# Kernel tuning notes

Hardware: AMD Instinct MI355X
Metric: run time of the kernel (lower is better)

Reference implementation:

```python
import jax, jax.numpy as jnp
import numpy as np

N_NODES = 50000
N_EDGES = 800000
D = 256          # in/out/hidden channels
F_EDGE = 64      # edge feature dim (edge_attr_dim - 1)
LN_EPS = 1e-5


def setup_inputs() -> dict:
    key = jax.random.key(0)
    ks = jax.random.split(key, 12)
    s = 0.05
    return {
        "x": jax.random.normal(ks[0], (N_NODES, D), jnp.float32),
        "edge_index": jax.random.randint(ks[1], (2, N_EDGES), 0, N_NODES, jnp.int64),
        "edge_attr": jax.random.normal(ks[2], (N_EDGES, F_EDGE + 1), jnp.float32),
        "W_e1": jax.random.normal(ks[3], (D, F_EDGE), jnp.float32) * s,
        "b_e1": jnp.zeros((D,), jnp.float32),
        "W_e2": jax.random.normal(ks[4], (D, D), jnp.float32) * s,
        "b_e2": jnp.zeros((D,), jnp.float32),
        "W_le": jax.random.normal(ks[5], (D, D), jnp.float32) * s,
        "b_le": jnp.zeros((D,), jnp.float32),
        "W_g1": jax.random.normal(ks[6], (D, D), jnp.float32) * s,
        "b_g1": jnp.zeros((D,), jnp.float32),
        "ln_g": jnp.ones((D,), jnp.float32),
        "ln_b": jnp.zeros((D,), jnp.float32),
        "W_g2": jax.random.normal(ks[7], (D, D), jnp.float32) * s,
        "b_g2": jnp.zeros((D,), jnp.float32),
    }


def reference(x, edge_index, edge_attr, W_e1, b_e1, W_e2, b_e2,
              W_le, b_le, W_g1, b_g1, ln_g, ln_b, W_g2, b_g2):
    # --- polarity gating + edge MLP (dropout = identity at inference) ---
    polarity = jnp.clip(edge_attr[:, 0:1], 0.0, 1.0)           # [E,1]
    raw = edge_attr[:, 1:]                                     # [E,F]
    e = jax.nn.relu(raw @ W_e1.T + b_e1) @ W_e2.T + b_e2       # [E,D]
    gated = e * (polarity + 0.01)                              # [E,D]
    # --- GINEConv: lin(edge) -> gather + add + relu -> scatter-sum ---
    edge_emb = gated @ W_le.T + b_le                           # [E,D]
    src, dst = edge_index[0], edge_index[1]
    msg = jax.nn.relu(x[src] + edge_emb)                       # [E,D]
    aggr = jax.ops.segment_sum(msg, dst, num_segments=x.shape[0])  # [N,D]
    # --- GIN MLP: Linear -> LayerNorm -> ReLU -> Linear (eps=0) ---
    h = (x + aggr) @ W_g1.T + b_g1                             # [N,D]
    mu = jnp.mean(h, axis=-1, keepdims=True)
    var = jnp.mean(jnp.square(h - mu), axis=-1, keepdims=True)
    hn = (h - mu) * jax.lax.rsqrt(var + LN_EPS) * ln_g + ln_b
    return jax.nn.relu(hn) @ W_g2.T + b_g2                     # [N,D]
```

## Files before the change

### kernel.cpp

```cpp
#include <hip/hip_runtime.h>
#include <stdint.h>

#define N_NODES 50000
#define N_EDGES 800000
#define DMODEL  256
#define FEDGE   64
#define TILE_E  64
#define N_ETILES (N_EDGES / TILE_E)
#define TILE_N  64
#define N_NTILES ((N_NODES + TILE_N - 1) / TILE_N)

typedef short short8 __attribute__((ext_vector_type(8)));
typedef float floatx4 __attribute__((ext_vector_type(4)));
typedef unsigned short ushort_t;
typedef unsigned short ushort4v __attribute__((ext_vector_type(4)));

__device__ __forceinline__ ushort_t f2bf(float f) {
  union { float f; unsigned int i; } v; v.f = f;
  unsigned int x = v.i;
  unsigned int r = x + 0x7fffu + ((x >> 16) & 1u);
  return (ushort_t)(r >> 16);
}
__device__ __forceinline__ short8 ldg16(const ushort_t* p) {
  return *(const short8*)(const void*)p;
}
__device__ __forceinline__ floatx4 ldf4(const float* p) {
  return *(const floatx4*)(const void*)p;
}

__global__ void prep_kernel(const float* __restrict__ W_le,
                            const float* __restrict__ W_e2,
                            const float* __restrict__ b_e2,
                            const float* __restrict__ W_e1,
                            const float* __restrict__ W_g1,
                            const float* __restrict__ W_g2,
                            ushort_t* __restrict__ Mw, float* __restrict__ cw,
                            ushort_t* __restrict__ We1bf,
                            ushort_t* __restrict__ Wg1bf,
                            ushort_t* __restrict__ Wg2bf) {
  int d = blockIdx.x, k = threadIdx.x;
  float acc = 0.f;
  for (int j = 0; j < DMODEL; ++j)
    acc += W_le[d * DMODEL + j] * W_e2[j * DMODEL + k];
  Mw[d * DMODEL + k] = f2bf(acc);
  Wg1bf[d * DMODEL + k] = f2bf(W_g1[d * DMODEL + k]);
  Wg2bf[d * DMODEL + k] = f2bf(W_g2[d * DMODEL + k]);
  if (k < FEDGE) We1bf[d * FEDGE + k] = f2bf(W_e1[d * FEDGE + k]);
  if (k == 0) {
    float cc = 0.f;
    for (int j = 0; j < DMODEL; ++j) cc += W_le[d * DMODEL + j] * b_e2[j];
    cw[d] = cc;
  }
}

__global__ void hist_kernel(const int* __restrict__ eidx, int* __restrict__ counts) {
  int e = blockIdx.x * blockDim.x + threadIdx.x;
  if (e < N_EDGES) atomicAdd(counts + eidx[N_EDGES + e], 1);
}

__global__ void scan_kernel(const int* __restrict__ counts, int* __restrict__ cur) {
  __shared__ int lds[1024];
  const int tid = threadIdx.x;
  int carry = 0;
  for (int base = 0; base < N_NODES; base += 1024) {
    int i = base + tid;
    int v = (i < N_NODES) ? counts[i] : 0;
    lds[tid] = v;
    __syncthreads();
#pragma unroll
    for (int off = 1; off < 1024; off <<= 1) {
      int t = (tid >= off) ? lds[tid - off] : 0;
      __syncthreads();
      lds[tid] += t;
      __syncthreads();
    }
    if (i < N_NODES) cur[i] = carry + lds[tid] - v;
    int tot = lds[1023];
    __syncthreads();
    carry += tot;
  }
}

__global__ void scatter_kernel(const int* __restrict__ eidx, int* __restrict__ cur,
                               int* __restrict__ perm) {
  int e = blockIdx.x * blockDim.x + threadIdx.x;
  if (e < N_EDGES) {
    int d = eidx[N_EDGES + e];
    int pos = atomicAdd(cur + d, 1);
    perm[pos] = e;
  }
}

__global__ __launch_bounds__(256, 3)
void edge_kernel(const float* __restrict__ x,
                 const int* __restrict__ eidx,
                 const float* __restrict__ eattr,
                 const int* __restrict__ perm,
                 const ushort_t* __restrict__ We1bf,
                 const float* __restrict__ b_e1,
                 const float* __restrict__ b_le,
                 const ushort_t* __restrict__ Mw,
                 const float* __restrict__ cw,
                 float* __restrict__ aggr) {
  __shared__ __align__(16) ushort_t raw_lds[TILE_E * 72];
  __shared__ __align__(16) ushort_t t1_lds[TILE_E * 264];
  __shared__ float pp_lds[TILE_E];
  __shared__ int src_lds[TILE_E];
  __shared__ int dst_lds[TILE_E + 1];

  const int tid  = threadIdx.x;
  const int lane = tid & 63;
  const int wave = tid >> 6;
  const int l16  = lane & 15;
  const int quad = lane >> 4;
  const int dbase = wave * 64;
  const long ebase = (long)blockIdx.x * TILE_E;

  {
    int r0 = tid >> 4, c = (tid & 15) * 4;
#pragma unroll
    for (int p = 0; p < 4; ++p) {
      int r = p * 16 + r0;
      int pe = perm[ebase + r];
      const float* sp = eattr + (long)pe * 65 + 1 + c;
      ushort4v pk = {f2bf(sp[0]), f2bf(sp[1]), f2bf(sp[2]), f2bf(sp[3])};
      *(ushort4v*)(void*)(raw_lds + r * 72 + c) = pk;
    }
    if (tid < TILE_E) {
      int pe = perm[ebase + tid];
      float pol = eattr[(long)pe * 65];
      pp_lds[tid] = fminf(fmaxf(pol, 0.f), 1.f) + 0.01f;
      src_lds[tid] = eidx[pe];
      dst_lds[tid] = eidx[N_EDGES + pe];
    }
    if (tid == 64) dst_lds[TILE_E] = -1;
  }
  __syncthreads();

  {
    floatx4 acc1[4][4];
#pragma unroll
    for (int m = 0; m < 4; ++m)
#pragma unroll
      for (int j = 0; j < 4; ++j) acc1[m][j] = (floatx4){0.f, 0.f, 0.f, 0.f};
#pragma unroll
    for (int kt = 0; kt < 2; ++kt) {
      short8 aW[4], bE[4];
#pragma unroll
      for (int m = 0; m < 4; ++m)
        aW[m] = ldg16(We1bf + (dbase + m * 16 + l16) * FEDGE + kt * 32 + quad * 8);
#pragma unroll
      for (int j = 0; j < 4; ++j)
        bE[j] = *(const short8*)(const void*)(raw_lds + (j * 16 + l16) * 72 + kt * 32 + quad * 8);
#pragma unroll
      for (int m = 0; m < 4; ++m)
#pragma unroll
        for (int j = 0; j < 4; ++j)
          acc1[m][j] = __builtin_amdgcn_mfma_f32_16x16x32_bf16(aW[m], bE[j], acc1[m][j], 0, 0, 0);
    }
#pragma unroll
    for (int m = 0; m < 4; ++m) {
      int f0 = dbase + m * 16 + quad * 4;
      floatx4 be1q = ldf4(b_e1 + f0);
#pragma unroll
      for (int j = 0; j < 4; ++j) {
        int e = j * 16 + l16;
        ushort4v pk = {f2bf(fmaxf(acc1[m][j][0] + be1q[0], 0.f)),
                       f2bf(fmaxf(acc1[m][j][1] + be1q[1], 0.f)),
                       f2bf(fmaxf(acc1[m][j][2] + be1q[2], 0.f)),
                       f2bf(fmaxf(acc1[m][j][3] + be1q[3], 0.f))};
        *(ushort4v*)(void*)(t1_lds + e * 264 + f0) = pk;
      }
    }
  }
  __syncthreads();

  floatx4 acc2[4][4];
#pragma unroll
  for (int m = 0; m < 4; ++m)
#pragma unroll
    for (int j = 0; j < 4; ++j) acc2[m][j] = (floatx4){0.f, 0.f, 0.f, 0.f};
#pragma unroll
  for (int kt = 0; kt < 8; ++kt) {
    short8 aW[4], bE[4];
#pragma unroll
    for (int m = 0; m < 4; ++m)
      aW[m] = ldg16(Mw + (dbase + m * 16 + l16) * DMODEL + kt * 32 + quad * 8);
#pragma unroll
    for (int j = 0; j < 4; ++j)
      bE[j] = *(const short8*)(const void*)(t1_lds + (j * 16 + l16) * 264 + kt * 32 + quad * 8);
#pragma unroll
    for (int m = 0; m < 4; ++m)
#pragma unroll
      for (int j = 0; j < 4; ++j)
        acc2[m][j] = __builtin_amdgcn_mfma_f32_16x16x32_bf16(aW[m], bE[j], acc2[m][j], 0, 0, 0);
  }
  __syncthreads();

  floatx4 cv4[4], blv4[4];
#pragma unroll
  for (int m = 0; m < 4; ++m) {
    int d0 = dbase + m * 16 + quad * 4;
    cv4[m] = ldf4(cw + d0);
    blv4[m] = ldf4(b_le + d0);
  }
  float* msgw = ((float*)(void*)t1_lds) + wave * (64 * 33);
  float runsum = 0.f;
  const int d_own = dbase + lane;

#pragma unroll
  for (int h = 0; h < 2; ++h) {
#pragma unroll
    for (int jj = 0; jj < 2; ++jj) {
      int j = h * 2 + jj;
      int e = j * 16 + l16;
      float pp = pp_lds[e];
      long srow = (long)src_lds[e] * DMODEL;
#pragma unroll
      for (int m = 0; m < 4; ++m) {
        int d0 = m * 16 + quad * 4;
        floatx4 xv = ldf4(x + srow + dbase + d0);
#pragma unroll
        for (int r = 0; r < 4; ++r)
          msgw[(d0 + r) * 33 + jj * 16 + l16] =
              fmaxf(xv[r] + pp * (acc2[m][j][r] + cv4[m][r]) + blv4[m][r], 0.f);
      }
    }
    __syncthreads();
    for (int el = 0; el < 32; ++el) {
      int eg = h * 32 + el;
      runsum += msgw[lane * 33 + el];
      if (dst_lds[eg] != dst_lds[eg + 1]) {
        atomicAdd(aggr + (long)dst_lds[eg] * DMODEL + d_own, runsum);
        runsum = 0.f;
      }
    }
    __syncthreads();
  }
}

__global__ __launch_bounds__(256, 3)
void node_kernel(const float* __restrict__ x,
                 const float* __restrict__ aggr,
                 const ushort_t* __restrict__ Wg1bf,
                 const float* __restrict__ b_g1,
                 const float* __restrict__ ln_g,
                 const float* __restrict__ ln_b,
                 const ushort_t* __restrict__ Wg2bf,
                 const float* __restrict__ b_g2,
                 float* __restrict__ out) {
  __shared__ __align__(16) ushort_t a_lds[TILE_N * 264];
  __shared__ float ws_s[4][TILE_N];
  __shared__ float ws_ss[4][TILE_N];
  __shared__ float mu_lds[TILE_N], rs_lds[TILE_N];

  const int tid  = threadIdx.x;
  const int lane = tid & 63;
  const int wave = tid >> 6;
  const int l16  = lane & 15;
  const int quad = lane >> 4;
  const int dbase = wave * 64;
  const long nbase = (long)blockIdx.x * TILE_N;

#pragma unroll
  for (int i = 0; i < 16; ++i) {
    int id = tid + 256 * i;
    int r = id >> 6, c4 = (id & 63) * 4;
    long rr = nbase + r; if (rr >= N_NODES) rr = N_NODES - 1;
    floatx4 xv = ldf4(x + rr * DMODEL + c4);
    floatx4 av = ldf4(aggr + rr * DMODEL + c4);
    ushort4v pk = {f2bf(xv[0] + av[0]), f2bf(xv[1] + av[1]),
                   f2bf(xv[2] + av[2]), f2bf(xv[3] + av[3])};
    *(ushort4v*)(void*)(a_lds + r * 264 + c4) = pk;
  }
  __syncthreads();

  floatx4 acc[4][4];
#pragma unroll
  for (int m = 0; m < 4; ++m)
#pragma unroll
    for (int j = 0; j < 4; ++j) acc[m][j] = (floatx4){0.f, 0.f, 0.f, 0.f};
#pragma unroll
  for (int kt = 0; kt < 8; ++kt) {
    short8 aW[4], bN[4];
#pragma unroll
    for (int m = 0; m < 4; ++m)
      aW[m] = ldg16(Wg1bf + (dbase + m * 16 + l16) * DMODEL + kt * 32 + quad * 8);
#pragma unroll
    for (int j = 0; j < 4; ++j)
      bN[j] = *(const short8*)(const void*)(a_lds + (j * 16 + l16) * 264 + kt * 32 + quad * 8);
#pragma unroll
    for (int m = 0; m < 4; ++m)
#pragma unroll
      for (int j = 0; j < 4; ++j)
        acc[m][j] = __builtin_amdgcn_mfma_f32_16x16x32_bf16(aW[m], bN[j], acc[m][j], 0, 0, 0);
  }
#pragma unroll
  for (int m = 0; m < 4; ++m) {
    floatx4 bq = ldf4(b_g1 + dbase + m * 16 + quad * 4);
#pragma unroll
    for (int j = 0; j < 4; ++j)
#pragma unroll
      for (int r = 0; r < 4; ++r) acc[m][j][r] += bq[r];
  }

#pragma unroll
  for (int j = 0; j < 4; ++j) {
    float s = 0.f, ss = 0.f;
#pragma unroll
    for (int m = 0; m < 4; ++m)
#pragma unroll
      for (int r = 0; r < 4; ++r) { float v = acc[m][j][r]; s += v; ss += v * v; }
    s += __shfl_xor(s, 16); ss += __shfl_xor(ss, 16);
    s += __shfl_xor(s, 32); ss += __shfl_xor(ss, 32);
    if (quad == 0) { ws_s[wave][j * 16 + l16] = s; ws_ss[wave][j * 16 + l16] = ss; }
  }
  __syncthreads();
  if (tid < TILE_N) {
    float s = ws_s[0][tid] + ws_s[1][tid] + ws_s[2][tid] + ws_s[3][tid];
    float ss = ws_ss[0][tid] + ws_ss[1][tid] + ws_ss[2][tid] + ws_ss[3][tid];
    float mu = s * (1.f / 256.f);
    float var = ss * (1.f / 256.f) - mu * mu;
    mu_lds[tid] = mu;
    rs_lds[tid] = rsqrtf(var + 1e-5f);
  }
  __syncthreads();

#pragma unroll
  for (int m = 0; m < 4; ++m) {
    int d0 = dbase + m * 16 + quad * 4;
    floatx4 lg = ldf4(ln_g + d0), lb = ldf4(ln_b + d0);
#pragma unroll
    for (int j = 0; j < 4; ++j) {
      int e = j * 16 + l16;
      float mu = mu_lds[e], rs = rs_lds[e];
      ushort4v pk = {f2bf(fmaxf((acc[m][j][0] - mu) * rs * lg[0] + lb[0], 0.f)),
                     f2bf(fmaxf((acc[m][j][1] - mu) * rs * lg[1] + lb[1], 0.f)),
                     f2bf(fmaxf((acc[m][j][2] - mu) * rs * lg[2] + lb[2], 0.f)),
                     f2bf(fmaxf((acc[m][j][3] - mu) * rs * lg[3] + lb[3], 0.f))};
      *(ushort4v*)(void*)(a_lds + e * 264 + d0) = pk;
    }
  }
  __syncthreads();

#pragma unroll
  for (int m = 0; m < 4; ++m)
#pragma unroll
    for (int j = 0; j < 4; ++j) acc[m][j] = (floatx4){0.f, 0.f, 0.f, 0.f};
#pragma unroll
  for (int kt = 0; kt < 8; ++kt) {
    short8 aW[4], bN[4];
#pragma unroll
    for (int m = 0; m < 4; ++m)
      aW[m] = ldg16(Wg2bf + (dbase + m * 16 + l16) * DMODEL + kt * 32 + quad * 8);
#pragma unroll
    for (int j = 0; j < 4; ++j)
      bN[j] = *(const short8*)(const void*)(a_lds + (j * 16 + l16) * 264 + kt * 32 + quad * 8);
#pragma unroll
    for (int m = 0; m < 4; ++m)
#pragma unroll
      for (int j = 0; j < 4; ++j)
        acc[m][j] = __builtin_amdgcn_mfma_f32_16x16x32_bf16(aW[m], bN[j], acc[m][j], 0, 0, 0);
  }
#pragma unroll
  for (int m = 0; m < 4; ++m) {
    int d0 = dbase + m * 16 + quad * 4;
    floatx4 bq = ldf4(b_g2 + d0);
#pragma unroll
    for (int j = 0; j < 4; ++j) {
      long row = nbase + j * 16 + l16;
      if (row < N_NODES) {
        floatx4 o = {acc[m][j][0] + bq[0], acc[m][j][1] + bq[1],
                     acc[m][j][2] + bq[2], acc[m][j][3] + bq[3]};
        *(floatx4*)(void*)(out + row * DMODEL + d0) = o;
      }
    }
  }
}

extern "C" void kernel_launch(void* const* d_in, const int* in_sizes, int n_in,
                              void* d_out, int out_size, void* d_ws, size_t ws_size,
                              hipStream_t stream) {
  const float* x     = (const float*)d_in[0];
  const int*   eidx  = (const int*)d_in[1];
  const float* eattr = (const float*)d_in[2];
  const float* W_e1  = (const float*)d_in[3];
  const float* b_e1  = (const float*)d_in[4];
  const float* W_e2  = (const float*)d_in[5];
  const float* b_e2  = (const float*)d_in[6];
  const float* W_le  = (const float*)d_in[7];
  const float* b_le  = (const float*)d_in[8];
  const float* W_g1  = (const float*)d_in[9];
  const float* b_g1  = (const float*)d_in[10];
  const float* ln_g  = (const float*)d_in[11];
  const float* ln_b  = (const float*)d_in[12];
  const float* W_g2  = (const float*)d_in[13];
  const float* b_g2  = (const float*)d_in[14];
  float* out = (float*)d_out;

  char* ws = (char*)d_ws;
  ushort_t* Mw     = (ushort_t*)(ws);
  ushort_t* Wg1bf  = (ushort_t*)(ws + 131072);
  ushort_t* Wg2bf  = (ushort_t*)(ws + 262144);
  ushort_t* We1bf  = (ushort_t*)(ws + 393216);
  float*    cw     = (float*)   (ws + 425984);
  float*    aggr   = (float*)   (ws + 427008);
  int*      counts = (int*)     (ws + 51627008);
  int*      cur    = (int*)     (ws + 51827008);
  int*      perm   = (int*)     (ws + 52027008);

  hipMemsetAsync(aggr, 0, (size_t)N_NODES * DMODEL * sizeof(float), stream);
  hipMemsetAsync(counts, 0, (size_t)N_NODES * sizeof(int), stream);
  prep_kernel<<<dim3(DMODEL), dim3(DMODEL), 0, stream>>>(
      W_le, W_e2, b_e2, W_e1, W_g1, W_g2, Mw, cw, We1bf, Wg1bf, Wg2bf);
  hist_kernel<<<dim3((N_EDGES + 255) / 256), dim3(256), 0, stream>>>(eidx, counts);
  scan_kernel<<<dim3(1), dim3(1024), 0, stream>>>(counts, cur);
  scatter_kernel<<<dim3((N_EDGES + 255) / 256), dim3(256), 0, stream>>>(eidx, cur, perm);
  edge_kernel<<<dim3(N_ETILES), dim3(256), 0, stream>>>(
      x, eidx, eattr, perm, We1bf, b_e1, b_le, Mw, cw, aggr);
  node_kernel<<<dim3(N_NTILES), dim3(256), 0, stream>>>(
      x, aggr, Wg1bf, b_g1, ln_g, ln_b, Wg2bf, b_g2, out);
}
```

Before: 972.7 us.

## Gather bf16 copy of x early, parallelize prefix scan across blocks

Adds a kernel that converts x to bf16 so the edge kernel's random per-edge row gather moves half the bytes. That gather is now issued before the edge MLP matmuls so its latency can overlap them, at the cost of extra registers. The single-block serial scan is replaced with a three-kernel, multi-block, wave-shuffle scan. The bf16 path runs only if the workspace is large enough and adds rounding error on x in the messages.

```diff
diff --git a/kernel.cpp b/kernel.cpp
--- a/kernel.cpp
+++ b/kernel.cpp
@@ -9,6 +9,7 @@
 #define N_ETILES (N_EDGES / TILE_E)
 #define TILE_N  64
 #define N_NTILES ((N_NODES + TILE_N - 1) / TILE_N)
+#define NB_SCAN ((N_NODES + 255) / 256)
 
 typedef short short8 __attribute__((ext_vector_type(8)));
 typedef float floatx4 __attribute__((ext_vector_type(4)));
@@ -20,6 +21,9 @@
   unsigned int x = v.i;
   unsigned int r = x + 0x7fffu + ((x >> 16) & 1u);
   return (ushort_t)(r >> 16);
+}
+__device__ __forceinline__ float bf2f(ushort_t u) {
+  union { unsigned int i; float f; } v; v.i = ((unsigned int)u) << 16; return v.f;
 }
 __device__ __forceinline__ short8 ldg16(const ushort_t* p) {
   return *(const short8*)(const void*)p;
@@ -53,32 +57,63 @@
   }
 }
 
+__global__ void xconv_kernel(const float* __restrict__ x, ushort_t* __restrict__ xbf) {
+  int i = blockIdx.x * blockDim.x + threadIdx.x;
+  floatx4 v = ldf4(x + (long)i * 4);
+  ushort4v pk = {f2bf(v[0]), f2bf(v[1]), f2bf(v[2]), f2bf(v[3])};
+  *(ushort4v*)(void*)(xbf + (long)i * 4) = pk;
+}
+
 __global__ void hist_kernel(const int* __restrict__ eidx, int* __restrict__ counts) {
   int e = blockIdx.x * blockDim.x + threadIdx.x;
   if (e < N_EDGES) atomicAdd(counts + eidx[N_EDGES + e], 1);
 }
 
-__global__ void scan_kernel(const int* __restrict__ counts, int* __restrict__ cur) {
-  __shared__ int lds[1024];
-  const int tid = threadIdx.x;
-  int carry = 0;
-  for (int base = 0; base < N_NODES; base += 1024) {
-    int i = base + tid;
-    int v = (i < N_NODES) ? counts[i] : 0;
-    lds[tid] = v;
-    __syncthreads();
-#pragma unroll
-    for (int off = 1; off < 1024; off <<= 1) {
-      int t = (tid >= off) ? lds[tid - off] : 0;
-      __syncthreads();
-      lds[tid] += t;
-      __syncthreads();
-    }
-    if (i < N_NODES) cur[i] = carry + lds[tid] - v;
-    int tot = lds[1023];
-    __syncthreads();
-    carry += tot;
-  }
+__global__ void scan_block_kernel(const int* __restrict__ counts,
+                                  int* __restrict__ cur, int* __restrict__ bsum) {
+  __shared__ int wsum[4];
+  int i = blockIdx.x * 256 + threadIdx.x;
+  int lane = threadIdx.x & 63, wave = threadIdx.x >> 6;
+  int v = (i < N_NODES) ? counts[i] : 0;
+  int s = v;
+#pragma unroll
+  for (int off = 1; off <= 32; off <<= 1) {
+    int t = __shfl_up(s, off);
+    if (lane >= off) s += t;
+  }
+  if (lane == 63) wsum[wave] = s;
+  __syncthreads();
+  int woff = 0;
+  if (wave > 0) woff += wsum[0];
+  if (wave > 1) woff += wsum[1];
+  if (wave > 2) woff += wsum[2];
+  if (i < N_NODES) cur[i] = s - v + woff;
+  if (threadIdx.x == 255) bsum[blockIdx.x] = s + woff;
+}
+
+__global__ void scan_total_kernel(const int* __restrict__ bsum, int* __restrict__ bofs) {
+  __shared__ int wsum[4];
+  int tid = threadIdx.x;
+  int lane = tid & 63, wave = tid >> 6;
+  int v = (tid < NB_SCAN) ? bsum[tid] : 0;
+  int s = v;
+#pragma unroll
+  for (int off = 1; off <= 32; off <<= 1) {
+    int t = __shfl_up(s, off);
+    if (lane >= off) s += t;
+  }
+  if (lane == 63) wsum[wave] = s;
+  __syncthreads();
+  int woff = 0;
+  if (wave > 0) woff += wsum[0];
+  if (wave > 1) woff += wsum[1];
+  if (wave > 2) woff += wsum[2];
+  if (tid < NB_SCAN) bofs[tid] = s - v + woff;
+}
+
+__global__ void scan_add_kernel(int* __restrict__ cur, const int* __restrict__ bofs) {
+  int i = blockIdx.x * 256 + threadIdx.x;
+  if (i < N_NODES) cur[i] += bofs[i >> 8];
 }
 
 __global__ void scatter_kernel(const int* __restrict__ eidx, int* __restrict__ cur,
@@ -91,8 +126,10 @@
   }
 }
 
+template <bool USEBF>
 __global__ __launch_bounds__(256, 3)
 void edge_kernel(const float* __restrict__ x,
+                 const ushort_t* __restrict__ xbf,
                  const int* __restrict__ eidx,
                  const float* __restrict__ eattr,
                  const int* __restrict__ perm,
@@ -137,6 +174,21 @@
   }
   __syncthreads();
 
+  ushort4v xpb[4][4];
+  floatx4  xpf[4][4];
+#pragma unroll
+  for (int j = 0; j < 4; ++j) {
+    long srow = (long)src_lds[j * 16 + l16] * DMODEL;
+#pragma unroll
+    for (int m = 0; m < 4; ++m) {
+      int d0 = dbase + m * 16 + quad * 4;
+      if constexpr (USEBF)
+        xpb[j][m] = *(const ushort4v*)(const void*)(xbf + srow + d0);
+      else
+        xpf[j][m] = ldf4(x + srow + d0);
+    }
+  }
+
   {
     floatx4 acc1[4][4];
 #pragma unroll
@@ -215,15 +267,21 @@
       int j = h * 2 + jj;
       int e = j * 16 + l16;
       float pp = pp_lds[e];
-      long srow = (long)src_lds[e] * DMODEL;
 #pragma unroll
       for (int m = 0; m < 4; ++m) {
         int d0 = m * 16 + quad * 4;
-        floatx4 xv = ldf4(x + srow + dbase + d0);
+        float xr[4];
+        if constexpr (USEBF) {
+#pragma unroll
+          for (int r = 0; r < 4; ++r) xr[r] = bf2f(xpb[j][m][r]);
+        } else {
+#pragma unroll
+          for (int r = 0; r < 4; ++r) xr[r] = xpf[j][m][r];
+        }
 #pragma unroll
         for (int r = 0; r < 4; ++r)
           msgw[(d0 + r) * 33 + jj * 16 + l16] =
-              fmaxf(xv[r] + pp * (acc2[m][j][r] + cv4[m][r]) + blv4[m][r], 0.f);
+              fmaxf(xr[r] + pp * (acc2[m][j][r] + cv4[m][r]) + blv4[m][r], 0.f);
       }
     }
     __syncthreads();
@@ -408,16 +466,29 @@
   int*      counts = (int*)     (ws + 51627008);
   int*      cur    = (int*)     (ws + 51827008);
   int*      perm   = (int*)     (ws + 52027008);
+  int*      bsum   = (int*)     (ws + 55227008);
+  int*      bofs   = (int*)     (ws + 55228032);
+  ushort_t* xbf    = (ushort_t*)(ws + 55229056);
+  const size_t NEED_BF = 80829056;
+  const bool use_bf = (ws_size >= NEED_BF);
 
   hipMemsetAsync(aggr, 0, (size_t)N_NODES * DMODEL * sizeof(float), stream);
   hipMemsetAsync(counts, 0, (size_t)N_NODES * sizeof(int), stream);
   prep_kernel<<<dim3(DMODEL), dim3(DMODEL), 0, stream>>>(
       W_le, W_e2, b_e2, W_e1, W_g1, W_g2, Mw, cw, We1bf, Wg1bf, Wg2bf);
+  if (use_bf)
+    xconv_kernel<<<dim3(N_NODES * DMODEL / 4 / 256), dim3(256), 0, stream>>>(x, xbf);
   hist_kernel<<<dim3((N_EDGES + 255) / 256), dim3(256), 0, stream>>>(eidx, counts);
-  scan_kernel<<<dim3(1), dim3(1024), 0, stream>>>(counts, cur);
+  scan_block_kernel<<<dim3(NB_SCAN), dim3(256), 0, stream>>>(counts, cur, bsum);
+  scan_total_kernel<<<dim3(1), dim3(256), 0, stream>>>(bsum, bofs);
+  scan_add_kernel<<<dim3(NB_SCAN), dim3(256), 0, stream>>>(cur, bofs);
   scatter_kernel<<<dim3((N_EDGES + 255) / 256), dim3(256), 0, stream>>>(eidx, cur, perm);
-  edge_kernel<<<dim3(N_ETILES), dim3(256), 0, stream>>>(
-      x, eidx, eattr, perm, We1bf, b_e1, b_le, Mw, cw, aggr);
+  if (use_bf)
+    edge_kernel<true><<<dim3(N_ETILES), dim3(256), 0, stream>>>(
+        x, xbf, eidx, eattr, perm, We1bf, b_e1, b_le, Mw, cw, aggr);
+  else
+    edge_kernel<false><<<dim3(N_ETILES), dim3(256), 0, stream>>>(
+        x, xbf, eidx, eattr, perm, We1bf, b_e1, b_le, Mw, cw, aggr);
   node_kernel<<<dim3(N_NTILES), dim3(256), 0, stream>>>(
       x, aggr, Wg1bf, b_g1, ln_g, ln_b, Wg2bf, b_g2, out);
 }
```

Result: faster. 952.4 us (-2.1%).
